# Performance work log

Measured on AMD Instinct MI355X. Metric: run time of the kernel, lower is better.

## Reference

```python
import jax, jax.numpy as jnp
import numpy as np

D_MODEL = 512
N_HEADS = 8
D_HEAD = D_MODEL // N_HEADS
EPS = 1e-6


def setup_inputs() -> dict:
    key = jax.random.key(0)
    ks = jax.random.split(key, 9)
    B, S = 2, 2048
    scale = 0.02
    x = jax.random.normal(ks[0], (B, S, D_MODEL), dtype=jnp.float32)
    Wq = jax.random.normal(ks[1], (D_MODEL, D_MODEL), dtype=jnp.float32) * scale
    Wk = jax.random.normal(ks[2], (D_MODEL, D_MODEL), dtype=jnp.float32) * scale
    Wv = jax.random.normal(ks[3], (D_MODEL, D_MODEL), dtype=jnp.float32) * scale
    Wo = jax.random.normal(ks[4], (D_MODEL, D_MODEL), dtype=jnp.float32) * scale
    bq = jax.random.normal(ks[5], (D_MODEL,), dtype=jnp.float32) * scale
    bk = jax.random.normal(ks[6], (D_MODEL,), dtype=jnp.float32) * scale
    bv = jax.random.normal(ks[7], (D_MODEL,), dtype=jnp.float32) * scale
    bo = jax.random.normal(ks[8], (D_MODEL,), dtype=jnp.float32) * scale
    return {"x": x, "Wq": Wq, "bq": bq, "Wk": Wk, "bk": bk,
            "Wv": Wv, "bv": bv, "Wo": Wo, "bo": bo}


def _split_heads(t, B, S):
    # [B,S,D] -> [B,H,S,dh]
    return t.reshape(B, S, N_HEADS, D_HEAD).transpose(0, 2, 1, 3)


def reference(x, Wq, bq, Wk, bk, Wv, bv, Wo, bo):
    B, S, _ = x.shape
    q = _split_heads(x @ Wq.T + bq, B, S)
    k = _split_heads(x @ Wk.T + bk, B, S)
    v = _split_heads(x @ Wv.T + bv, B, S)
    # 'relu' kernel applied to Q and K
    q = jax.nn.relu(q)
    k = jax.nn.relu(k)
    # K_sum: [B,H,S,1] -- per-position sum over head dim; note it broadcasts
    # over the KEY axis of attn, i.e. each QUERY row n is divided by K_sum[n]
    k_sum = k.sum(axis=-1, keepdims=True)
    attn = jnp.einsum('bhnd,bhmd->bhnm', q, k) / (k_sum + EPS)
    attn = jax.nn.softmax(attn, axis=-1)
    out = jnp.einsum('bhnm,bhmd->bhnd', attn, v)
    out = out.transpose(0, 2, 1, 3).reshape(B, S, D_MODEL)
    return (out @ Wo.T + bo, attn)
```

## Files before the change

### kernel.cpp

```cpp
#include <hip/hip_runtime.h>
#include <stdint.h>


typedef __attribute__((ext_vector_type(8))) short short8;
typedef __attribute__((ext_vector_type(4))) float f4;

#define MFMA(a, b, c) __builtin_amdgcn_mfma_f32_16x16x32_bf16(a, b, c, 0, 0, 0)

struct __align__(8) us4 { uint16_t a, b, c, d; };

__device__ __forceinline__ uint16_t f2bf(float f) {
  union { float f; uint32_t u; } v; v.f = f;
  uint32_t u = v.u;
  return (uint16_t)((u + 0x7fffu + ((u >> 16) & 1u)) >> 16);
}
__device__ __forceinline__ float bf2f(uint16_t u) {
  union { uint32_t u; float f; } v; v.u = ((uint32_t)u) << 16; return v.f;
}
__device__ __forceinline__ us4 pack4(float4 v) {
  us4 r; r.a = f2bf(v.x); r.b = f2bf(v.y); r.c = f2bf(v.z); r.d = f2bf(v.w); return r;
}

__device__ __forceinline__ void async16(const uint16_t* g, uint16_t* l) {
  __builtin_amdgcn_global_load_lds(
      (const __attribute__((address_space(1))) void*)g,
      (__attribute__((address_space(3))) void*)l, 16, 0, 0);
}

__global__ __launch_bounds__(256) void convert_kernel(
    const float* __restrict__ x, const float* __restrict__ Wq,
    const float* __restrict__ Wk, const float* __restrict__ Wv,
    const float* __restrict__ Wo, uint16_t* __restrict__ xb,
    uint16_t* __restrict__ W3, uint16_t* __restrict__ Wob) {
  int i = blockIdx.x * 256 + threadIdx.x;
  ((us4*)xb)[i] = pack4(((const float4*)x)[i]);
  if (i < 65536) {
    ((us4*)W3)[i]           = pack4(((const float4*)Wq)[i]);
    ((us4*)W3)[65536 + i]   = pack4(((const float4*)Wk)[i]);
    ((us4*)W3)[131072 + i]  = pack4(((const float4*)Wv)[i]);
    ((us4*)Wob)[i]          = pack4(((const float4*)Wo)[i]);
  }
}

__device__ __forceinline__ void gemm_loop(
    const uint16_t* __restrict__ A, const uint16_t* __restrict__ Bt,
    int row0, int col0, uint16_t* Alds, uint16_t* Blds, f4 (&acc)[4][4]) {
  const int tid = threadIdx.x;
  const int w = tid >> 6, lane = tid & 63;
  const int c = lane & 15, quad = lane >> 4;
  const int wm = w >> 1, wn = w & 1;
  const int srow = lane >> 2, scol = (lane & 3) * 8;
  const uint16_t* Asrc = A + (size_t)(row0 + srow) * 512 + scol;
  const uint16_t* Bsrc = Bt + (size_t)(col0 + srow) * 512 + scol;
  for (int k0 = 0; k0 < 512; k0 += 32) {
    __syncthreads();
#pragma unroll
    for (int chh = 0; chh < 2; ++chh) {
      int ch = w * 2 + chh;
      async16(Asrc + (size_t)ch * 16 * 512 + k0, Alds + ch * 512);
      async16(Bsrc + (size_t)ch * 16 * 512 + k0, Blds + ch * 512);
    }
    __syncthreads();
    short8 af[4], bf[4];
#pragma unroll
    for (int mi = 0; mi < 4; ++mi)
      af[mi] = *(const short8*)&Alds[(wm * 64 + mi * 16 + c) * 32 + quad * 8];
#pragma unroll
    for (int ni = 0; ni < 4; ++ni)
      bf[ni] = *(const short8*)&Blds[(wn * 64 + ni * 16 + c) * 32 + quad * 8];
#pragma unroll
    for (int mi = 0; mi < 4; ++mi)
#pragma unroll
      for (int ni = 0; ni < 4; ++ni)
        acc[mi][ni] = MFMA(af[mi], bf[ni], acc[mi][ni]);
  }
}

__global__ __launch_bounds__(256) void qkv_gemm(
    const uint16_t* __restrict__ xb, const uint16_t* __restrict__ W3,
    const float* __restrict__ bq, const float* __restrict__ bk,
    const float* __restrict__ bv, uint16_t* __restrict__ Qb,
    uint16_t* __restrict__ Kb, uint16_t* __restrict__ Vt) {
  __shared__ __align__(16) uint16_t Alds[128 * 32];
  __shared__ __align__(16) uint16_t Blds[128 * 32];
  f4 acc[4][4] = {};
  const int row0 = blockIdx.y * 128, col0 = blockIdx.x * 128;
  gemm_loop(xb, W3, row0, col0, Alds, Blds, acc);
  const int tid = threadIdx.x, w = tid >> 6, lane = tid & 63;
  const int c = lane & 15, quad = lane >> 4;
  const int wm = w >> 1, wn = w & 1;
  const int r3 = col0 >> 9;
  const float* bias = (r3 == 0) ? bq : (r3 == 1) ? bk : bv;
#pragma unroll
  for (int mi = 0; mi < 4; ++mi)
#pragma unroll
    for (int ni = 0; ni < 4; ++ni)
#pragma unroll
      for (int r = 0; r < 4; ++r) {
        int row = row0 + wm * 64 + mi * 16 + quad * 4 + r;
        int col = col0 + wn * 64 + ni * 16 + c;
        int o = col & 511;
        float v = acc[mi][ni][r] + bias[o];
        if (r3 == 0) {
          Qb[(size_t)row * 512 + o] = f2bf(fmaxf(v, 0.0f));
        } else if (r3 == 1) {
          Kb[(size_t)row * 512 + o] = f2bf(fmaxf(v, 0.0f));
        } else {
          int h = o >> 6, d = o & 63;
          int b = row >> 11, s = row & 2047;
          Vt[((size_t)(b * 8 + h) * 64 + d) * 2048 + s] = f2bf(v);
        }
      }
}

__global__ __launch_bounds__(256) void proj_gemm(
    const uint16_t* __restrict__ Ob, const uint16_t* __restrict__ Wob,
    const float* __restrict__ bo, float* __restrict__ out) {
  __shared__ __align__(16) uint16_t Alds[128 * 32];
  __shared__ __align__(16) uint16_t Blds[128 * 32];
  f4 acc[4][4] = {};
  const int row0 = blockIdx.y * 128, col0 = blockIdx.x * 128;
  gemm_loop(Ob, Wob, row0, col0, Alds, Blds, acc);
  const int tid = threadIdx.x, w = tid >> 6, lane = tid & 63;
  const int c = lane & 15, quad = lane >> 4;
  const int wm = w >> 1, wn = w & 1;
#pragma unroll
  for (int mi = 0; mi < 4; ++mi)
#pragma unroll
    for (int ni = 0; ni < 4; ++ni)
#pragma unroll
      for (int r = 0; r < 4; ++r) {
        int row = row0 + wm * 64 + mi * 16 + quad * 4 + r;
        int col = col0 + wn * 64 + ni * 16 + c;
        out[(size_t)row * 512 + col] = acc[mi][ni][r] + bo[col];
      }
}

__global__ __launch_bounds__(256) void ksum_kernel(
    const uint16_t* __restrict__ Kb, float* __restrict__ rq) {
  int i = blockIdx.x * 256 + threadIdx.x;
  const uint16_t* p = Kb + (size_t)i * 64;
  float s = 0.f;
#pragma unroll
  for (int j = 0; j < 64; ++j) s += bf2f(p[j]);
  rq[i] = 1.0f / (s + 1e-6f);
}

__global__ __launch_bounds__(256) void attn_kernel(
    const uint16_t* __restrict__ Qb, const uint16_t* __restrict__ Kb,
    const uint16_t* __restrict__ Vt, const float* __restrict__ rq,
    float* __restrict__ attn, uint16_t* __restrict__ Ob) {
  __shared__ __align__(16) uint16_t Klds[64 * 64];
  __shared__ __align__(16) uint16_t Vlds[64 * 64];
  __shared__ __align__(16) uint16_t Plds[4][16 * 64];
  const int tid = threadIdx.x, w = tid >> 6, lane = tid & 63;
  const int c = lane & 15, quad = lane >> 4;
  const int bh = blockIdx.y, b = bh >> 3, h = bh & 7;
  const int n0 = blockIdx.x * 64;
  const int rbase = b * 2048 + n0;
  const uint16_t* qptr = Qb + (size_t)(rbase + w * 16 + c) * 512 + h * 64 + quad * 8;
  short8 aq0 = *(const short8*)qptr;
  short8 aq1 = *(const short8*)(qptr + 32);
  float rqv[4];
#pragma unroll
  for (int r = 0; r < 4; ++r)
    rqv[r] = rq[(size_t)(rbase + w * 16 + quad * 4 + r) * 8 + h];
  const int srow = lane >> 3, scol = (lane & 7) * 8;
  const uint16_t* Ksrc = Kb + (size_t)(b * 2048) * 512 + h * 64 + scol;
  const uint16_t* Vsrc = Vt + (size_t)bh * 64 * 2048 + scol;

  float lsum[4] = {0.f, 0.f, 0.f, 0.f};
  for (int kt = 0; kt < 32; ++kt) {
    __syncthreads();
#pragma unroll
    for (int chh = 0; chh < 2; ++chh) {
      int ch = w * 2 + chh;
      async16(Ksrc + (size_t)(kt * 64 + ch * 8 + srow) * 512, Klds + ch * 512);
    }
    __syncthreads();
#pragma unroll
    for (int ni = 0; ni < 4; ++ni) {
      const uint16_t* kp = &Klds[(ni * 16 + c) * 64 + quad * 8];
      short8 bk0 = *(const short8*)kp;
      short8 bk1 = *(const short8*)(kp + 32);
      f4 s = {};
      s = MFMA(aq0, bk0, s);
      s = MFMA(aq1, bk1, s);
#pragma unroll
      for (int r = 0; r < 4; ++r) lsum[r] += __expf(s[r] * rqv[r]);
    }
  }
  float rli[4];
#pragma unroll
  for (int r = 0; r < 4; ++r) {
    float v = lsum[r];
    v += __shfl_xor(v, 1, 16);
    v += __shfl_xor(v, 2, 16);
    v += __shfl_xor(v, 4, 16);
    v += __shfl_xor(v, 8, 16);
    rli[r] = 1.0f / v;
  }

  f4 oacc[4] = {};
  float* arow = attn + ((size_t)bh * 2048 + n0 + w * 16) * 2048;
  for (int kt = 0; kt < 32; ++kt) {
    __syncthreads();
#pragma unroll
    for (int chh = 0; chh < 2; ++chh) {
      int ch = w * 2 + chh;
      async16(Ksrc + (size_t)(kt * 64 + ch * 8 + srow) * 512, Klds + ch * 512);
      async16(Vsrc + (size_t)(ch * 8 + srow) * 2048 + kt * 64, Vlds + ch * 512);
    }
    __syncthreads();
#pragma unroll
    for (int ni = 0; ni < 4; ++ni) {
      const uint16_t* kp = &Klds[(ni * 16 + c) * 64 + quad * 8];
      short8 bk0 = *(const short8*)kp;
      short8 bk1 = *(const short8*)(kp + 32);
      f4 s = {};
      s = MFMA(aq0, bk0, s);
      s = MFMA(aq1, bk1, s);
#pragma unroll
      for (int r = 0; r < 4; ++r) {
        float p = __expf(s[r] * rqv[r]) * rli[r];
        arow[(size_t)(quad * 4 + r) * 2048 + kt * 64 + ni * 16 + c] = p;
        Plds[w][(quad * 4 + r) * 64 + ni * 16 + c] = f2bf(p);
      }
    }
    asm volatile("s_waitcnt lgkmcnt(0)" ::: "memory");
#pragma unroll
    for (int ks = 0; ks < 2; ++ks) {
      short8 ap = *(const short8*)&Plds[w][c * 64 + ks * 32 + quad * 8];
#pragma unroll
      for (int nj = 0; nj < 4; ++nj) {
        short8 bvv = *(const short8*)&Vlds[(nj * 16 + c) * 64 + ks * 32 + quad * 8];
        oacc[nj] = MFMA(ap, bvv, oacc[nj]);
      }
    }
  }
#pragma unroll
  for (int nj = 0; nj < 4; ++nj)
#pragma unroll
    for (int r = 0; r < 4; ++r)
      Ob[(size_t)(rbase + w * 16 + quad * 4 + r) * 512 + h * 64 + nj * 16 + c] =
          f2bf(oacc[nj][r]);
}

extern "C" void kernel_launch(void* const* d_in, const int* in_sizes, int n_in,
                              void* d_out, int out_size, void* d_ws, size_t ws_size,
                              hipStream_t stream) {
  const float* x  = (const float*)d_in[0];
  const float* Wq = (const float*)d_in[1];
  const float* bq = (const float*)d_in[2];
  const float* Wk = (const float*)d_in[3];
  const float* bk = (const float*)d_in[4];
  const float* Wv = (const float*)d_in[5];
  const float* bv = (const float*)d_in[6];
  const float* Wo = (const float*)d_in[7];
  const float* bo = (const float*)d_in[8];

  float* out0 = (float*)d_out;
  float* attn = out0 + (size_t)2 * 2048 * 512;

  uint8_t* ws = (uint8_t*)d_ws;
  uint16_t* xb  = (uint16_t*)(ws);
  uint16_t* W3  = (uint16_t*)(ws + 0x400000);
  uint16_t* Wob = (uint16_t*)(ws + 0x580000);
  uint16_t* Qb  = (uint16_t*)(ws + 0x600000);
  uint16_t* Kb  = (uint16_t*)(ws + 0xA00000);
  uint16_t* Vt  = (uint16_t*)(ws + 0xE00000);
  uint16_t* Ob  = (uint16_t*)(ws + 0x1200000);
  float*    rq  = (float*)  (ws + 0x1600000);

  convert_kernel<<<2048, 256, 0, stream>>>(x, Wq, Wk, Wv, Wo, xb, W3, Wob);
  qkv_gemm<<<dim3(12, 32), 256, 0, stream>>>(xb, W3, bq, bk, bv, Qb, Kb, Vt);
  ksum_kernel<<<128, 256, 0, stream>>>(Kb, rq);
  attn_kernel<<<dim3(32, 16), 256, 0, stream>>>(Qb, Kb, Vt, rq, attn, Ob);
  proj_gemm<<<dim3(4, 32), 256, 0, stream>>>(Ob, Wob, bo, out0);
}
```

Before: 409.0 us.

## Swizzle LDS layouts, stage attn writes through LDS, transpose V via shared tile

Applies XOR swizzles to the LDS tiles in the GEMM loop and the attention K/V tiles to avoid bank conflicts. The attention probability tile is staged in fp32 LDS so each lane writes the attn matrix with 16-byte row-contiguous stores instead of scattered scalar stores. The V transpose in the QKV epilogue goes through a shared tile for coalesced writes, and the ksum kernel uses vector loads with a shuffle reduction. The attention grid is also remapped so blocks are ordered by head. This raises LDS use, which may reduce occupancy.

```diff
diff --git a/kernel.cpp b/kernel.cpp
--- a/kernel.cpp
+++ b/kernel.cpp
@@ -35,10 +35,10 @@
   int i = blockIdx.x * 256 + threadIdx.x;
   ((us4*)xb)[i] = pack4(((const float4*)x)[i]);
   if (i < 65536) {
-    ((us4*)W3)[i]           = pack4(((const float4*)Wq)[i]);
-    ((us4*)W3)[65536 + i]   = pack4(((const float4*)Wk)[i]);
-    ((us4*)W3)[131072 + i]  = pack4(((const float4*)Wv)[i]);
-    ((us4*)Wob)[i]          = pack4(((const float4*)Wo)[i]);
+    ((us4*)W3)[i]          = pack4(((const float4*)Wq)[i]);
+    ((us4*)W3)[65536 + i]  = pack4(((const float4*)Wk)[i]);
+    ((us4*)W3)[131072 + i] = pack4(((const float4*)Wv)[i]);
+    ((us4*)Wob)[i]         = pack4(((const float4*)Wo)[i]);
   }
 }
 
@@ -49,9 +49,11 @@
   const int w = tid >> 6, lane = tid & 63;
   const int c = lane & 15, quad = lane >> 4;
   const int wm = w >> 1, wn = w & 1;
-  const int srow = lane >> 2, scol = (lane & 3) * 8;
-  const uint16_t* Asrc = A + (size_t)(row0 + srow) * 512 + scol;
-  const uint16_t* Bsrc = Bt + (size_t)(col0 + srow) * 512 + scol;
+  const int srow = lane >> 2;
+  const int sslot = ((lane & 3) ^ ((lane >> 2) & 3) ^ ((lane >> 4) & 3)) * 8;
+  const uint16_t* Asrc = A + (size_t)(row0 + srow) * 512 + sslot;
+  const uint16_t* Bsrc = Bt + (size_t)(col0 + srow) * 512 + sslot;
+  const int posv = (quad ^ (c & 3) ^ (c >> 2)) * 8;
   for (int k0 = 0; k0 < 512; k0 += 32) {
     __syncthreads();
 #pragma unroll
@@ -64,10 +66,10 @@
     short8 af[4], bf[4];
 #pragma unroll
     for (int mi = 0; mi < 4; ++mi)
-      af[mi] = *(const short8*)&Alds[(wm * 64 + mi * 16 + c) * 32 + quad * 8];
+      af[mi] = *(const short8*)&Alds[(wm * 64 + mi * 16 + c) * 32 + posv];
 #pragma unroll
     for (int ni = 0; ni < 4; ++ni)
-      bf[ni] = *(const short8*)&Blds[(wn * 64 + ni * 16 + c) * 32 + quad * 8];
+      bf[ni] = *(const short8*)&Blds[(wn * 64 + ni * 16 + c) * 32 + posv];
 #pragma unroll
     for (int mi = 0; mi < 4; ++mi)
 #pragma unroll
@@ -83,6 +85,7 @@
     uint16_t* __restrict__ Kb, uint16_t* __restrict__ Vt) {
   __shared__ __align__(16) uint16_t Alds[128 * 32];
   __shared__ __align__(16) uint16_t Blds[128 * 32];
+  __shared__ __align__(16) uint16_t Ct[128 * 136];
   f4 acc[4][4] = {};
   const int row0 = blockIdx.y * 128, col0 = blockIdx.x * 128;
   gemm_loop(xb, W3, row0, col0, Alds, Blds, acc);
@@ -90,27 +93,47 @@
   const int c = lane & 15, quad = lane >> 4;
   const int wm = w >> 1, wn = w & 1;
   const int r3 = col0 >> 9;
-  const float* bias = (r3 == 0) ? bq : (r3 == 1) ? bk : bv;
-#pragma unroll
-  for (int mi = 0; mi < 4; ++mi)
-#pragma unroll
-    for (int ni = 0; ni < 4; ++ni)
-#pragma unroll
-      for (int r = 0; r < 4; ++r) {
-        int row = row0 + wm * 64 + mi * 16 + quad * 4 + r;
-        int col = col0 + wn * 64 + ni * 16 + c;
-        int o = col & 511;
-        float v = acc[mi][ni][r] + bias[o];
-        if (r3 == 0) {
-          Qb[(size_t)row * 512 + o] = f2bf(fmaxf(v, 0.0f));
-        } else if (r3 == 1) {
-          Kb[(size_t)row * 512 + o] = f2bf(fmaxf(v, 0.0f));
-        } else {
-          int h = o >> 6, d = o & 63;
-          int b = row >> 11, s = row & 2047;
-          Vt[((size_t)(b * 8 + h) * 64 + d) * 2048 + s] = f2bf(v);
+  if (r3 < 2) {
+    const float* bias = (r3 == 0) ? bq : bk;
+    uint16_t* dst = (r3 == 0) ? Qb : Kb;
+#pragma unroll
+    for (int mi = 0; mi < 4; ++mi)
+#pragma unroll
+      for (int ni = 0; ni < 4; ++ni)
+#pragma unroll
+        for (int r = 0; r < 4; ++r) {
+          int row = row0 + wm * 64 + mi * 16 + quad * 4 + r;
+          int col = col0 + wn * 64 + ni * 16 + c;
+          int o = col & 511;
+          float v = acc[mi][ni][r] + bias[o];
+          dst[(size_t)row * 512 + o] = f2bf(fmaxf(v, 0.0f));
         }
-      }
+  } else {
+#pragma unroll
+    for (int mi = 0; mi < 4; ++mi)
+#pragma unroll
+      for (int ni = 0; ni < 4; ++ni)
+#pragma unroll
+        for (int r = 0; r < 4; ++r) {
+          int sl = wm * 64 + mi * 16 + quad * 4 + r;
+          int cl = wn * 64 + ni * 16 + c;
+          int o = (col0 + cl) & 511;
+          Ct[sl * 136 + cl] = f2bf(acc[mi][ni][r] + bv[o]);
+        }
+    __syncthreads();
+    const int b = row0 >> 11, s0 = row0 & 2047;
+    const int cl = tid >> 1, half = tid & 1;
+    const int ocol = (col0 - 1024) + cl;
+    uint16_t* vdst = Vt + (size_t)(b * 512 + ocol) * 2048 + s0 + half * 64;
+#pragma unroll
+    for (int g = 0; g < 8; ++g) {
+      union { short8 v; uint16_t e[8]; } o8;
+#pragma unroll
+      for (int jj = 0; jj < 8; ++jj)
+        o8.e[jj] = Ct[(half * 64 + g * 8 + jj) * 136 + cl];
+      *(short8*)(vdst + g * 8) = o8.v;
+    }
+  }
 }
 
 __global__ __launch_bounds__(256) void proj_gemm(
@@ -138,12 +161,19 @@
 
 __global__ __launch_bounds__(256) void ksum_kernel(
     const uint16_t* __restrict__ Kb, float* __restrict__ rq) {
-  int i = blockIdx.x * 256 + threadIdx.x;
-  const uint16_t* p = Kb + (size_t)i * 64;
+  int t = blockIdx.x * 256 + threadIdx.x;
+  int row = t >> 2, part = t & 3;
+  const uint4* p = (const uint4*)(Kb + (size_t)row * 64 + part * 16);
   float s = 0.f;
 #pragma unroll
-  for (int j = 0; j < 64; ++j) s += bf2f(p[j]);
-  rq[i] = 1.0f / (s + 1e-6f);
+  for (int g = 0; g < 2; ++g) {
+    union { uint4 u; uint16_t e[8]; } v; v.u = p[g];
+#pragma unroll
+    for (int j = 0; j < 8; ++j) s += bf2f(v.e[j]);
+  }
+  s += __shfl_xor(s, 1, 4);
+  s += __shfl_xor(s, 2, 4);
+  if (part == 0) rq[row] = 1.0f / (s + 1e-6f);
 }
 
 __global__ __launch_bounds__(256) void attn_kernel(
@@ -152,11 +182,14 @@
     float* __restrict__ attn, uint16_t* __restrict__ Ob) {
   __shared__ __align__(16) uint16_t Klds[64 * 64];
   __shared__ __align__(16) uint16_t Vlds[64 * 64];
-  __shared__ __align__(16) uint16_t Plds[4][16 * 64];
+  __shared__ __align__(16) float Pw[4][16 * 64];
   const int tid = threadIdx.x, w = tid >> 6, lane = tid & 63;
-  const int c = lane & 15, quad = lane >> 4;
-  const int bh = blockIdx.y, b = bh >> 3, h = bh & 7;
-  const int n0 = blockIdx.x * 64;
+  const int c = lane & 15, quad = lane >> 4, c7 = c & 7;
+  const int bid = blockIdx.x;
+  const int bh = (bid & 7) * 2 + ((bid >> 3) & 1);
+  const int qt = bid >> 4;
+  const int b = bh >> 3, h = bh & 7;
+  const int n0 = qt * 64;
   const int rbase = b * 2048 + n0;
   const uint16_t* qptr = Qb + (size_t)(rbase + w * 16 + c) * 512 + h * 64 + quad * 8;
   short8 aq0 = *(const short8*)qptr;
@@ -165,9 +198,10 @@
 #pragma unroll
   for (int r = 0; r < 4; ++r)
     rqv[r] = rq[(size_t)(rbase + w * 16 + quad * 4 + r) * 8 + h];
-  const int srow = lane >> 3, scol = (lane & 7) * 8;
-  const uint16_t* Ksrc = Kb + (size_t)(b * 2048) * 512 + h * 64 + scol;
-  const uint16_t* Vsrc = Vt + (size_t)bh * 64 * 2048 + scol;
+  const int vsrow = lane >> 3;
+  const int vslot = ((lane & 7) ^ vsrow) * 8;
+  const uint16_t* Ksrc = Kb + (size_t)(b * 2048) * 512 + h * 64 + vslot;
+  const uint16_t* Vsrc = Vt + (size_t)(bh * 64) * 2048 + vslot;
 
   float lsum[4] = {0.f, 0.f, 0.f, 0.f};
   for (int kt = 0; kt < 32; ++kt) {
@@ -175,14 +209,14 @@
 #pragma unroll
     for (int chh = 0; chh < 2; ++chh) {
       int ch = w * 2 + chh;
-      async16(Ksrc + (size_t)(kt * 64 + ch * 8 + srow) * 512, Klds + ch * 512);
+      async16(Ksrc + (size_t)(kt * 64 + ch * 8 + vsrow) * 512, Klds + ch * 512);
     }
     __syncthreads();
 #pragma unroll
     for (int ni = 0; ni < 4; ++ni) {
-      const uint16_t* kp = &Klds[(ni * 16 + c) * 64 + quad * 8];
-      short8 bk0 = *(const short8*)kp;
-      short8 bk1 = *(const short8*)(kp + 32);
+      const uint16_t* kp = &Klds[(ni * 16 + c) * 64];
+      short8 bk0 = *(const short8*)(kp + ((quad ^ c7) * 8));
+      short8 bk1 = *(const short8*)(kp + (((quad + 4) ^ c7) * 8));
       f4 s = {};
       s = MFMA(aq0, bk0, s);
       s = MFMA(aq1, bk1, s);
@@ -202,39 +236,48 @@
   }
 
   f4 oacc[4] = {};
-  float* arow = attn + ((size_t)bh * 2048 + n0 + w * 16) * 2048;
+  float* arowc = attn + ((size_t)bh * 2048 + n0 + w * 16 + c) * 2048;
+  float* Pme = Pw[w];
   for (int kt = 0; kt < 32; ++kt) {
     __syncthreads();
 #pragma unroll
     for (int chh = 0; chh < 2; ++chh) {
       int ch = w * 2 + chh;
-      async16(Ksrc + (size_t)(kt * 64 + ch * 8 + srow) * 512, Klds + ch * 512);
-      async16(Vsrc + (size_t)(ch * 8 + srow) * 2048 + kt * 64, Vlds + ch * 512);
+      async16(Ksrc + (size_t)(kt * 64 + ch * 8 + vsrow) * 512, Klds + ch * 512);
+      async16(Vsrc + (size_t)(ch * 8 + vsrow) * 2048 + kt * 64, Vlds + ch * 512);
     }
     __syncthreads();
 #pragma unroll
     for (int ni = 0; ni < 4; ++ni) {
-      const uint16_t* kp = &Klds[(ni * 16 + c) * 64 + quad * 8];
-      short8 bk0 = *(const short8*)kp;
-      short8 bk1 = *(const short8*)(kp + 32);
+      const uint16_t* kp = &Klds[(ni * 16 + c) * 64];
+      short8 bk0 = *(const short8*)(kp + ((quad ^ c7) * 8));
+      short8 bk1 = *(const short8*)(kp + (((quad + 4) ^ c7) * 8));
       f4 s = {};
       s = MFMA(aq0, bk0, s);
       s = MFMA(aq1, bk1, s);
 #pragma unroll
       for (int r = 0; r < 4; ++r) {
+        int rowp = quad * 4 + r;
         float p = __expf(s[r] * rqv[r]) * rli[r];
-        arow[(size_t)(quad * 4 + r) * 2048 + kt * 64 + ni * 16 + c] = p;
-        Plds[w][(quad * 4 + r) * 64 + ni * 16 + c] = f2bf(p);
+        Pme[rowp * 64 + (((ni * 4 + (c >> 2)) ^ rowp) * 4) + (c & 3)] = p;
       }
     }
     asm volatile("s_waitcnt lgkmcnt(0)" ::: "memory");
 #pragma unroll
     for (int ks = 0; ks < 2; ++ks) {
-      short8 ap = *(const short8*)&Plds[w][c * 64 + ks * 32 + quad * 8];
+      int ch0 = ks * 8 + quad * 2;
+      f4 p0 = *(const f4*)&Pme[c * 64 + ((ch0 ^ c) * 4)];
+      f4 p1 = *(const f4*)&Pme[c * 64 + (((ch0 + 1) ^ c) * 4)];
+      *(f4*)&arowc[kt * 64 + ch0 * 4] = p0;
+      *(f4*)&arowc[kt * 64 + ch0 * 4 + 4] = p1;
+      union { short8 v; uint16_t e[8]; } ap;
+#pragma unroll
+      for (int i = 0; i < 4; ++i) { ap.e[i] = f2bf(p0[i]); ap.e[4 + i] = f2bf(p1[i]); }
 #pragma unroll
       for (int nj = 0; nj < 4; ++nj) {
-        short8 bvv = *(const short8*)&Vlds[(nj * 16 + c) * 64 + ks * 32 + quad * 8];
-        oacc[nj] = MFMA(ap, bvv, oacc[nj]);
+        short8 bvv = *(const short8*)&Vlds[(nj * 16 + c) * 64 +
+                                           (((ks * 4 + quad) ^ c7) * 8)];
+        oacc[nj] = MFMA(ap.v, bvv, oacc[nj]);
       }
     }
   }
@@ -274,7 +317,7 @@
 
   convert_kernel<<<2048, 256, 0, stream>>>(x, Wq, Wk, Wv, Wo, xb, W3, Wob);
   qkv_gemm<<<dim3(12, 32), 256, 0, stream>>>(xb, W3, bq, bk, bv, Qb, Kb, Vt);
-  ksum_kernel<<<128, 256, 0, stream>>>(Kb, rq);
-  attn_kernel<<<dim3(32, 16), 256, 0, stream>>>(Qb, Kb, Vt, rq, attn, Ob);
+  ksum_kernel<<<512, 256, 0, stream>>>(Kb, rq);
+  attn_kernel<<<512, 256, 0, stream>>>(Qb, Kb, Vt, rq, attn, Ob);
   proj_gemm<<<dim3(4, 32), 256, 0, stream>>>(Ob, Wob, bo, out0);
 }
```

Measured after the change: 386.0 us. 5.6% less time.
